# Kernel tuning notes

Measured on AMD Instinct MI355X. Metric: run time of the kernel, lower is better.

## Reference

```python
import jax, jax.numpy as jnp
import numpy as np

D = 64          # graph size d
HID = 1024      # hidden_dim of drift/diffusion MLPs


def _mlp(A_flat, t_val, W1, b1, W2, b2):
    """MLP over flattened adjacency concatenated with scalar time. A_flat: (..., d*d)."""
    t_col = jnp.full(A_flat.shape[:-1] + (1,), t_val, dtype=A_flat.dtype)
    x = jnp.concatenate([A_flat, t_col], axis=-1)          # (..., d*d+1)
    h = jnp.tanh(x @ W1 + b1)                              # (..., HID)
    return h @ W2 + b2                                     # (..., d*d)


def setup_inputs() -> dict:
    key = jax.random.key(0)
    ks = jax.random.split(key, 12)
    B, T = 64, 64
    A0 = jax.random.normal(ks[0], (B, D, D), dtype=jnp.float32)
    t = jnp.arange(T, dtype=jnp.float32) * 0.01
    din = D * D + 1
    s1 = 1.0 / np.sqrt(din)
    s2 = 1.0 / np.sqrt(HID)
    W1f = jax.random.normal(ks[1], (din, HID), jnp.float32) * s1
    b1f = jnp.zeros((HID,), jnp.float32)
    W2f = jax.random.normal(ks[2], (HID, D * D), jnp.float32) * s2
    b2f = jnp.zeros((D * D,), jnp.float32)
    W1g = jax.random.normal(ks[3], (din, HID), jnp.float32) * s1
    b1g = jnp.zeros((HID,), jnp.float32)
    W2g = jax.random.normal(ks[4], (HID, D * D), jnp.float32) * s2
    b2g = jnp.zeros((D * D,), jnp.float32)
    return dict(A0=A0, t=t, W1f=W1f, b1f=b1f, W2f=W2f, b2f=b2f,
                W1g=W1g, b1g=b1g, W2g=W2g, b2g=b2g, num_samples=4)


def reference(A0, t, W1f, b1f, W2f, b2f, W1g, b1g, W2g, b2g, num_samples):
    S = num_samples
    B = A0.shape[0]
    T = t.shape[0]
    dt = t[1] - t[0]
    sqrt_dt = jnp.sqrt(dt)
    A_init = jnp.broadcast_to(A0[None], (S, B, D, D))
    noise_keys = jax.random.split(jax.random.key(42), T - 1)

    def step(A_prev, inp):
        t_prev, k = inp
        Af = A_prev.reshape(S, B, D * D)
        drift = _mlp(Af, t_prev, W1f, b1f, W2f, b2f).reshape(S, B, D, D)
        diffusion = jax.nn.softplus(_mlp(Af, t_prev, W1g, b1g, W2g, b2g)).reshape(S, B, D, D)
        # torch draws dW with shape (*batch, d, d): shared across num_samples
        dW = jax.random.normal(k, (B, D, D), dtype=A_prev.dtype) * sqrt_dt
        A_next = A_prev + drift * dt + diffusion * dW
        return A_next, A_next

    _, traj = jax.lax.scan(step, A_init, (t[:-1], noise_keys))   # (T-1, S, B, d, d)
    A = jnp.concatenate([A_init[None], traj], axis=0)            # (T, S, B, d, d)
    A = jnp.swapaxes(A, 0, 1)                                    # (S, T, B, d, d)
    # ThresholdedSigmoid in training mode + zeroed diagonal
    G = jax.nn.sigmoid(A) * (1.0 - jnp.eye(D, dtype=A.dtype))
    return G
```

## Files before the change

### kernel.cpp

```cpp
#include <hip/hip_runtime.h>
#include <cstdint>

using u16 = unsigned short;
using u32 = uint32_t;
using u64 = unsigned long long;

typedef __bf16 bf16x8 __attribute__((ext_vector_type(8)));
typedef float  f32x4  __attribute__((ext_vector_type(4)));
typedef u32    uvec4  __attribute__((ext_vector_type(4)));

typedef const __attribute__((address_space(1))) void GV;
typedef __attribute__((address_space(3))) void LV;

#define MFMA(a, b, c) __builtin_amdgcn_mfma_f32_16x16x32_bf16((a), (b), (c), 0, 0, 0)
#define SCOPE_AGT __HIP_MEMORY_SCOPE_AGENT

static __device__ __forceinline__ void gl_lds16(const u16* g, u16* l) {
  __builtin_amdgcn_global_load_lds((GV*)g, (LV*)l, 16, 0, 0);
}
static __device__ __forceinline__ void st_dev(u64* p, u64 v) {
  __hip_atomic_store(p, v, __ATOMIC_RELAXED, SCOPE_AGT);
}

static __device__ __forceinline__ u16 f2bf(float x) {
  u32 u = __float_as_uint(x);
  u32 r = (u + 0x7FFFu + ((u >> 16) & 1u)) >> 16;
  return (u16)r;
}

static __device__ __forceinline__ u32 rotl32(u32 v, int s) {
  return (v << s) | (v >> (32 - s));
}

static __device__ __forceinline__ void threefry2x32(u32 k0, u32 k1, u32 x0, u32 x1,
                                                    u32& o0, u32& o1) {
  u32 k2 = k0 ^ k1 ^ 0x1BD11BDAu;
  x0 += k0; x1 += k1;
  x0 += x1; x1 = rotl32(x1, 13); x1 ^= x0;
  x0 += x1; x1 = rotl32(x1, 15); x1 ^= x0;
  x0 += x1; x1 = rotl32(x1, 26); x1 ^= x0;
  x0 += x1; x1 = rotl32(x1, 6);  x1 ^= x0;
  x0 += k1; x1 += k2 + 1u;
  x0 += x1; x1 = rotl32(x1, 17); x1 ^= x0;
  x0 += x1; x1 = rotl32(x1, 29); x1 ^= x0;
  x0 += x1; x1 = rotl32(x1, 16); x1 ^= x0;
  x0 += x1; x1 = rotl32(x1, 24); x1 ^= x0;
  x0 += k2; x1 += k0 + 2u;
  x0 += x1; x1 = rotl32(x1, 13); x1 ^= x0;
  x0 += x1; x1 = rotl32(x1, 15); x1 ^= x0;
  x0 += x1; x1 = rotl32(x1, 26); x1 ^= x0;
  x0 += x1; x1 = rotl32(x1, 6);  x1 ^= x0;
  x0 += k0; x1 += k1 + 3u;
  x0 += x1; x1 = rotl32(x1, 17); x1 ^= x0;
  x0 += x1; x1 = rotl32(x1, 29); x1 ^= x0;
  x0 += x1; x1 = rotl32(x1, 16); x1 ^= x0;
  x0 += x1; x1 = rotl32(x1, 24); x1 ^= x0;
  x0 += k1; x1 += k2 + 4u;
  x0 += x1; x1 = rotl32(x1, 13); x1 ^= x0;
  x0 += x1; x1 = rotl32(x1, 15); x1 ^= x0;
  x0 += x1; x1 = rotl32(x1, 26); x1 ^= x0;
  x0 += x1; x1 = rotl32(x1, 6);  x1 ^= x0;
  x0 += k2; x1 += k0 + 5u;
  o0 = x0; o1 = x1;
}

static __device__ __forceinline__ float bits_to_normal(u32 bits) {
  const float lo = __uint_as_float(0xBF7FFFFFu);
  float f = __uint_as_float((bits >> 9) | 0x3F800000u) - 1.0f;
  float x = fmaxf(lo, f * 2.0f + lo);
  float w = -logf((1.0f - x) * (1.0f + x));
  float p;
  if (w < 5.0f) {
    w -= 2.5f;
    p = 2.81022636e-08f;
    p = fmaf(p, w, 3.43273939e-07f);
    p = fmaf(p, w, -3.5233877e-06f);
    p = fmaf(p, w, -4.39150654e-06f);
    p = fmaf(p, w, 0.00021858087f);
    p = fmaf(p, w, -0.00125372503f);
    p = fmaf(p, w, -0.00417768164f);
    p = fmaf(p, w, 0.246640727f);
    p = fmaf(p, w, 1.50140941f);
  } else {
    w = sqrtf(w) - 3.0f;
    p = -0.000200214257f;
    p = fmaf(p, w, 0.000100950558f);
    p = fmaf(p, w, 0.00134934322f);
    p = fmaf(p, w, -0.00367342844f);
    p = fmaf(p, w, 0.00573950773f);
    p = fmaf(p, w, -0.0076224613f);
    p = fmaf(p, w, 0.00943887047f);
    p = fmaf(p, w, 1.00167406f);
    p = fmaf(p, w, 2.83297682f);
  }
  return 1.41421356f * p * x;
}

__global__ __launch_bounds__(256) void s1_frag(
    const float* __restrict__ W1f, const float* __restrict__ W1g,
    const float* __restrict__ W2f, const float* __restrict__ W2g,
    u16* __restrict__ W1P, u16* __restrict__ W2P) {
  const int gid = blockIdx.x * 256 + threadIdx.x;
  const int f = gid >> 6, l = gid & 63;
  const int lr = l & 15, kg = l >> 4;
  u32 wbuf[4];
  if (f < 16384) {
    const int net = f >> 13, r = f & 8191, ct = r >> 7, q = r & 127;
    const float* __restrict__ src = net ? W1g : W1f;
    const int k = q * 32 + kg * 8, c = ct * 16 + lr;
    #pragma unroll
    for (int p = 0; p < 4; ++p) {
      u16 e0 = f2bf(src[(size_t)(k + 2 * p) * 1024 + c]);
      u16 e1 = f2bf(src[(size_t)(k + 2 * p + 1) * 1024 + c]);
      wbuf[p] = (u32)e0 | ((u32)e1 << 16);
    }
    *(uvec4*)(W1P + (size_t)f * 512 + l * 8) = *(uvec4*)wbuf;
  } else {
    const int f2 = f - 16384;
    const int net = f2 >> 13, r = f2 & 8191, ct = r >> 5, q = r & 31;
    const float* __restrict__ src = net ? W2g : W2f;
    const int k = q * 32 + kg * 8, c = ct * 16 + lr;
    #pragma unroll
    for (int p = 0; p < 4; ++p) {
      u16 e0 = f2bf(src[(size_t)(k + 2 * p) * 4096 + c]);
      u16 e1 = f2bf(src[(size_t)(k + 2 * p + 1) * 4096 + c]);
      wbuf[p] = (u32)e0 | ((u32)e1 << 16);
    }
    *(uvec4*)(W2P + (size_t)f2 * 512 + l * 8) = *(uvec4*)wbuf;
  }
}

__global__ __launch_bounds__(256) void s2_init(
    const float* __restrict__ A0, u16* __restrict__ APack,
    u32* __restrict__ ctr, float* __restrict__ out) {
  const int gid = blockIdx.x * 256 + threadIdx.x;
  const int n = gid & 4095, b = gid >> 12;
  const float a0 = A0[gid];
  const float sig = (n % 65 == 0) ? 0.0f : 1.0f / (1.0f + expf(-a0));
  #pragma unroll
  for (int s = 0; s < 4; ++s)
    out[((size_t)(s * 64) * 64 + b) * 4096 + n] = sig;
  if (gid < 32768) {
    const int fr = gid >> 6, l = gid & 63;
    const int m = fr >> 7, q = fr & 127;
    const int row = m * 16 + (l & 15);
    const int k = q * 32 + (l >> 4) * 8;
    u32 wbuf[4];
    #pragma unroll
    for (int p = 0; p < 4; ++p) {
      u16 e0 = f2bf(A0[(size_t)row * 4096 + k + 2 * p]);
      u16 e1 = f2bf(A0[(size_t)row * 4096 + k + 2 * p + 1]);
      wbuf[p] = (u32)e0 | ((u32)e1 << 16);
    }
    *(uvec4*)(APack + (size_t)fr * 512 + l * 8) = *(uvec4*)wbuf;
  }
  if (gid < 2048) ctr[gid] = 0;
}

static __device__ __forceinline__ void half_barrier(u32* ctr, int mp, int g, u32 tag) {
  __syncthreads();
  if (threadIdx.x == 0) {
    u32* arr  = ctr + (mp * 20 + g) * 32;
    u32* glob = ctr + (mp * 20 + 8) * 32;
    u32* flg  = ctr + (mp * 20 + 9 + g) * 32;
    u32 old = __hip_atomic_fetch_add(arr, 1u, __ATOMIC_RELAXED, SCOPE_AGT);
    if (old + 1u == 16u * tag) {
      u32 go = __hip_atomic_fetch_add(glob, 1u, __ATOMIC_RELAXED, SCOPE_AGT);
      if (go + 1u == 8u * tag) {
        #pragma unroll
        for (int i = 0; i < 8; ++i)
          __hip_atomic_store(ctr + (mp * 20 + 9 + i) * 32, tag, __ATOMIC_RELAXED, SCOPE_AGT);
      }
    }
    while (__hip_atomic_load(flg, __ATOMIC_RELAXED, SCOPE_AGT) < tag)
      __builtin_amdgcn_s_sleep(8);
  }
  __syncthreads();
}

__global__ __launch_bounds__(512) void sde_fused(
    const float* __restrict__ A0, const float* __restrict__ tarr,
    const u16* __restrict__ W1P, const u16* __restrict__ W2P,
    const float* __restrict__ b1f, const float* __restrict__ b1g,
    const float* __restrict__ W1fv, const float* __restrict__ W1gv,
    const float* __restrict__ b2f, const float* __restrict__ b2g,
    u16* __restrict__ APack, u16* __restrict__ HPack,
    u32* __restrict__ ctr, float* __restrict__ out) {
  extern __shared__ __align__(16) char smraw[];
  u16* w2l = (u16*)smraw;
  char* exraw = smraw + 131072;
  f32x4 (*paex)[64]     = (f32x4 (*)[64])exraw;
  u16 (*patile)[16][16] = (u16 (*)[16][16])(exraw + 8192);
  f32x4 (*pbex)[64][2]  = (f32x4 (*)[64][2])exraw;
  u16 (*pbtile)[16][32] = (u16 (*)[16][32])(exraw + 16384);
  uint2* dwk = (uint2*)(exraw + 18432);

  const int bid = blockIdx.x, tix = threadIdx.x;
  const int wid = tix >> 6, lane = tix & 63;
  const int lr = lane & 15, lq = lane >> 4;
  const int mp = bid >> 7;
  const int ctF = bid & 127;
  const int netA = ctF >> 6, ctA = ctF & 63;
  const int mA = wid & 1, ksA = wid >> 1;
  const int mGA = mp * 2 + mA;
  const int ct32 = bid & 127;
  const int ksB = wid >> 2, netB = (wid >> 1) & 1, mB = wid & 1;
  const int mGB = mp * 2 + mB;
  const int eM = wid & 1, eCf = (wid >> 1) & 1, eRh = wid >> 2;
  const int nc = ct32 * 32 + eCf * 16 + lr;
  const int g = (bid & 127) >> 4;

  #pragma unroll
  for (int i = 0; i < 16; ++i) {
    const int f = wid * 16 + i;
    const int nf = f >> 6, cf = (f >> 5) & 1, ksf = (f >> 4) & 1, df = f & 15;
    const u16* src = W2P
        + ((size_t)((nf * 256 + ct32 * 2 + cf) * 32 + ksf * 16 + df)) * 512 + lane * 8;
    gl_lds16(src, w2l + (size_t)f * 512);
  }
  if (tix < 63) {
    u32 y0, y1;
    threefry2x32(0u, 42u, 0u, (u32)tix, y0, y1);
    dwk[tix] = make_uint2(y0, y1);
  }
  bf16x8 wv[32];
  {
    const u16* pw = W1P + ((size_t)((netA * 64 + ctA) * 128 + ksA * 32)) * 512 + lane * 8;
    #pragma unroll
    for (int d = 0; d < 32; ++d) wv[d] = *(const bf16x8*)(pw + (size_t)d * 512);
  }
  float Ast[2];
  #pragma unroll
  for (int ri = 0; ri < 2; ++ri) {
    const int row = mp * 32 + eM * 16 + lq * 4 + eRh * 2 + ri;
    Ast[ri] = A0[(size_t)row * 4096 + nc];
  }
  asm volatile("s_waitcnt vmcnt(0)" ::: "memory");
  __syncthreads();

  const float dt = tarr[1] - tarr[0];
  const float sdt = sqrtf(dt);

  for (int step = 0; step < 63; ++step) {
    {
      const u16* pa = APack + (size_t)step * 262144
                    + ((size_t)(mGA * 128 + ksA * 32)) * 512 + lane * 8;
      bf16x8 av[16];
      #pragma unroll
      for (int d = 0; d < 16; ++d) av[d] = *(const bf16x8*)(pa + (size_t)d * 512);
      f32x4 acc = {0.f, 0.f, 0.f, 0.f};
      #pragma unroll
      for (int j = 0; j < 32; ++j) {
        const int s = j & 15;
        acc = MFMA(av[s], wv[j], acc);
        if (j + 16 < 32) av[s] = *(const bf16x8*)(pa + (size_t)(j + 16) * 512);
      }
      paex[wid][lane] = acc;
      __syncthreads();
      {
        const int gM = wid & 1, gR = wid >> 1;
        const f32x4 s0 = paex[gM][lane];
        const f32x4 s1 = paex[2 + gM][lane];
        const f32x4 s2 = paex[4 + gM][lane];
        const f32x4 s3 = paex[6 + gM][lane];
        const float ch = s0[gR] + s1[gR] + s2[gR] + s3[gR];
        const int ncl = ctA * 16 + lr;
        const float* __restrict__ b1 = netA ? b1g : b1f;
        const float* __restrict__ wl = (netA ? W1gv : W1fv) + (size_t)4096 * 1024;
        const float cc = b1[ncl] + tarr[step] * wl[ncl];
        patile[gM][lq * 4 + gR][lr] = f2bf(tanhf(ch + cc));
      }
      __syncthreads();
      if (wid < 2 && lane < 32) {
        const int mm = wid;
        const int row = lane & 15, kp = lane >> 4;
        const u16* src = &patile[mm][row][kp * 8];
        const u64 lo = *(const u64*)src;
        const u64 hi = *(const u64*)(src + 4);
        const int k8 = (ctA & 1) * 2 + kp;
        u16* dst = HPack + (size_t)step * 131072
                 + ((size_t)((netA * 4 + mp * 2 + mm) * 32 + (ctA >> 1))) * 512
                 + (k8 * 16 + row) * 8;
        st_dev((u64*)dst, lo);
        st_dev((u64*)dst + 1, hi);
      }
      asm volatile("s_waitcnt vmcnt(0)" ::: "memory");
      half_barrier(ctr, mp, g, 2u * (u32)step + 1u);
    }

    {
      const u16* ph = HPack + (size_t)step * 131072
                    + ((size_t)((netB * 4 + mGB) * 32 + ksB * 16)) * 512 + lane * 8;
      bf16x8 hv[8];
      #pragma unroll
      for (int d = 0; d < 8; ++d) hv[d] = *(const bf16x8*)(ph + (size_t)d * 512);
      const u16* wl0 = w2l + (size_t)(netB * 64 + ksB * 16) * 512 + lane * 8;
      const u16* wl1 = wl0 + (size_t)32 * 512;
      f32x4 a0 = {0.f, 0.f, 0.f, 0.f}, a1 = a0;
      #pragma unroll
      for (int j = 0; j < 16; ++j) {
        const int s = j & 7;
        const bf16x8 w0 = *(const bf16x8*)(wl0 + (size_t)j * 512);
        const bf16x8 w1 = *(const bf16x8*)(wl1 + (size_t)j * 512);
        a0 = MFMA(hv[s], w0, a0);
        a1 = MFMA(hv[s], w1, a1);
        if (j + 8 < 16) hv[s] = *(const bf16x8*)(ph + (size_t)(j + 8) * 512);
      }
      pbex[wid][lane][0] = a0;
      pbex[wid][lane][1] = a1;
      __syncthreads();
      float sg[2];
      {
        const f32x4 CF = pbex[eM][lane][eCf] + pbex[4 + eM][lane][eCf];
        const f32x4 CG = pbex[2 + eM][lane][eCf] + pbex[6 + eM][lane][eCf];
        const float bfv = b2f[nc], bgv = b2g[nc];
        const uint2 key = dwk[step];
        #pragma unroll
        for (int ri = 0; ri < 2; ++ri) {
          const int r = eRh * 2 + ri;
          const int row = mp * 32 + eM * 16 + lq * 4 + r;
          const float drift = CF[r] + bfv;
          const float graw = CG[r] + bgv;
          const float diff = fmaxf(graw, 0.0f) + log1pf(expf(-fabsf(graw)));
          u32 y0, y1;
          threefry2x32(key.x, key.y, 0u, (u32)(row * 4096 + nc), y0, y1);
          const float dw = bits_to_normal(y0 ^ y1) * sdt;
          const float an = Ast[ri] + drift * dt + diff * dw;
          Ast[ri] = an;
          pbtile[eM][lq * 4 + r][eCf * 16 + lr] = f2bf(an);
          sg[ri] = (nc % 65 == 0) ? 0.0f : 1.0f / (1.0f + expf(-an));
        }
      }
      __syncthreads();
      if (wid < 2) {
        const int mm = wid;
        const int row = lane & 15, kq = lane >> 4;
        const u16* src = &pbtile[mm][row][kq * 8];
        const u64 lo = *(const u64*)src;
        const u64 hi = *(const u64*)(src + 4);
        u16* dst = APack + (size_t)(step + 1) * 262144
                 + ((size_t)((mp * 2 + mm) * 128 + ct32)) * 512 + lane * 8;
        st_dev((u64*)dst, lo);
        st_dev((u64*)dst + 1, hi);
      }
      asm volatile("s_waitcnt vmcnt(0)" ::: "memory");
      #pragma unroll
      for (int ri = 0; ri < 2; ++ri) {
        const int row = mp * 32 + eM * 16 + lq * 4 + eRh * 2 + ri;
        #pragma unroll
        for (int s = 0; s < 4; ++s)
          __builtin_nontemporal_store(
              sg[ri], &out[((size_t)(s * 64 + step + 1) * 64 + row) * 4096 + nc]);
      }
      if (step < 62) half_barrier(ctr, mp, g, 2u * (u32)step + 2u);
    }
  }
}

extern "C" void kernel_launch(void* const* d_in, const int* in_sizes, int n_in,
                              void* d_out, int out_size, void* d_ws, size_t ws_size,
                              hipStream_t stream) {
  const float* A0 = (const float*)d_in[0];
  const float* tarr = (const float*)d_in[1];
  const float* W1f = (const float*)d_in[2];
  const float* b1f = (const float*)d_in[3];
  const float* W2f = (const float*)d_in[4];
  const float* b2f = (const float*)d_in[5];
  const float* W1g = (const float*)d_in[6];
  const float* b1g = (const float*)d_in[7];
  const float* W2g = (const float*)d_in[8];
  const float* b2g = (const float*)d_in[9];
  float* outp = (float*)d_out;
  char* ws = (char*)d_ws;
  const size_t MB = 1024 * 1024;
  u16* W1P   = (u16*)(ws + 0 * MB);
  u16* W2P   = (u16*)(ws + 16 * MB);
  u16* APack = (u16*)(ws + 32 * MB);
  u16* HPack = (u16*)(ws + 64 * MB);
  u32* ctr   = (u32*)(ws + 80 * MB);

  s1_frag<<<dim3(8192), 256, 0, stream>>>(W1f, W1g, W2f, W2g, W1P, W2P);
  s2_init<<<dim3(1024), 256, 0, stream>>>(A0, APack, ctr, outp);

  void* kargs[] = {
    (void*)&A0, (void*)&tarr,
    (void*)&W1P, (void*)&W2P,
    (void*)&b1f, (void*)&b1g, (void*)&W1f, (void*)&W1g,
    (void*)&b2f, (void*)&b2g,
    (void*)&APack, (void*)&HPack, (void*)&ctr, (void*)&outp
  };
  hipLaunchCooperativeKernel((const void*)sde_fused, dim3(256), dim3(512),
                             kargs, 150016, stream);
}
```

Measured before the change: 795.9 us.

## Replace group barriers with per-dependency counters and split MFMA accumulators

Drops the two-level half_barrier. Each block now bumps an arrival counter after publishing its tile, and before the next phase it waits only on the two counters for the producer groups whose data it actually reads. Output stores are moved after the arrival signal, the per-step bias and time-weight loads are hoisted out of the loop, and the first GEMM alternates between two accumulators to shorten the MFMA dependency chain. The intent is to cut global synchronisation latency and let blocks run ahead, but correctness now rests on the counter indexing and memory ordering being exact.

```diff
diff --git a/kernel.cpp b/kernel.cpp
--- a/kernel.cpp
+++ b/kernel.cpp
@@ -20,6 +20,12 @@
 }
 static __device__ __forceinline__ void st_dev(u64* p, u64 v) {
   __hip_atomic_store(p, v, __ATOMIC_RELAXED, SCOPE_AGT);
+}
+static __device__ __forceinline__ void wait_pair(const u32* base, u32 tag) {
+  while (__hip_atomic_load(base, __ATOMIC_RELAXED, SCOPE_AGT) < tag)
+    __builtin_amdgcn_s_sleep(2);
+  while (__hip_atomic_load(base + 32, __ATOMIC_RELAXED, SCOPE_AGT) < tag)
+    __builtin_amdgcn_s_sleep(2);
 }
 
 static __device__ __forceinline__ u16 f2bf(float x) {
@@ -157,27 +163,6 @@
   if (gid < 2048) ctr[gid] = 0;
 }
 
-static __device__ __forceinline__ void half_barrier(u32* ctr, int mp, int g, u32 tag) {
-  __syncthreads();
-  if (threadIdx.x == 0) {
-    u32* arr  = ctr + (mp * 20 + g) * 32;
-    u32* glob = ctr + (mp * 20 + 8) * 32;
-    u32* flg  = ctr + (mp * 20 + 9 + g) * 32;
-    u32 old = __hip_atomic_fetch_add(arr, 1u, __ATOMIC_RELAXED, SCOPE_AGT);
-    if (old + 1u == 16u * tag) {
-      u32 go = __hip_atomic_fetch_add(glob, 1u, __ATOMIC_RELAXED, SCOPE_AGT);
-      if (go + 1u == 8u * tag) {
-        #pragma unroll
-        for (int i = 0; i < 8; ++i)
-          __hip_atomic_store(ctr + (mp * 20 + 9 + i) * 32, tag, __ATOMIC_RELAXED, SCOPE_AGT);
-      }
-    }
-    while (__hip_atomic_load(flg, __ATOMIC_RELAXED, SCOPE_AGT) < tag)
-      __builtin_amdgcn_s_sleep(8);
-  }
-  __syncthreads();
-}
-
 __global__ __launch_bounds__(512) void sde_fused(
     const float* __restrict__ A0, const float* __restrict__ tarr,
     const u16* __restrict__ W1P, const u16* __restrict__ W2P,
@@ -208,7 +193,11 @@
   const int mGB = mp * 2 + mB;
   const int eM = wid & 1, eCf = (wid >> 1) & 1, eRh = wid >> 2;
   const int nc = ct32 * 32 + eCf * 16 + lr;
-  const int g = (bid & 127) >> 4;
+  const int g = ctF >> 4;
+  u32* arrA = ctr + (mp * 8 + g) * 32;
+  u32* arrB = ctr + (16 + mp * 8 + g) * 32;
+  const u32* waitA = ctr + (16 + mp * 8 + ksA * 2) * 32;
+  const u32* waitB = ctr + (mp * 8 + netB * 4 + ksB * 2) * 32;
 
   #pragma unroll
   for (int i = 0; i < 16; ++i) {
@@ -235,6 +224,11 @@
     const int row = mp * 32 + eM * 16 + lq * 4 + eRh * 2 + ri;
     Ast[ri] = A0[(size_t)row * 4096 + nc];
   }
+  const int nclA = ctA * 16 + lr;
+  const float bAc = (netA ? b1g : b1f)[nclA];
+  const float wAc = ((netA ? W1gv : W1fv) + (size_t)4096 * 1024)[nclA];
+  const float bfv = b2f[nc], bgv = b2g[nc];
+  const bool diag0 = (nc % 65 == 0);
   asm volatile("s_waitcnt vmcnt(0)" ::: "memory");
   __syncthreads();
 
@@ -243,19 +237,21 @@
 
   for (int step = 0; step < 63; ++step) {
     {
+      wait_pair(waitA, 16u * (u32)step);
       const u16* pa = APack + (size_t)step * 262144
                     + ((size_t)(mGA * 128 + ksA * 32)) * 512 + lane * 8;
       bf16x8 av[16];
       #pragma unroll
       for (int d = 0; d < 16; ++d) av[d] = *(const bf16x8*)(pa + (size_t)d * 512);
-      f32x4 acc = {0.f, 0.f, 0.f, 0.f};
+      f32x4 acc0 = {0.f, 0.f, 0.f, 0.f}, acc1 = acc0;
       #pragma unroll
       for (int j = 0; j < 32; ++j) {
         const int s = j & 15;
-        acc = MFMA(av[s], wv[j], acc);
+        if (j & 1) acc1 = MFMA(av[s], wv[j], acc1);
+        else       acc0 = MFMA(av[s], wv[j], acc0);
         if (j + 16 < 32) av[s] = *(const bf16x8*)(pa + (size_t)(j + 16) * 512);
       }
-      paex[wid][lane] = acc;
+      paex[wid][lane] = acc0 + acc1;
       __syncthreads();
       {
         const int gM = wid & 1, gR = wid >> 1;
@@ -264,10 +260,7 @@
         const f32x4 s2 = paex[4 + gM][lane];
         const f32x4 s3 = paex[6 + gM][lane];
         const float ch = s0[gR] + s1[gR] + s2[gR] + s3[gR];
-        const int ncl = ctA * 16 + lr;
-        const float* __restrict__ b1 = netA ? b1g : b1f;
-        const float* __restrict__ wl = (netA ? W1gv : W1fv) + (size_t)4096 * 1024;
-        const float cc = b1[ncl] + tarr[step] * wl[ncl];
+        const float cc = bAc + tarr[step] * wAc;
         patile[gM][lq * 4 + gR][lr] = f2bf(tanhf(ch + cc));
       }
       __syncthreads();
@@ -285,10 +278,13 @@
         st_dev((u64*)dst + 1, hi);
       }
       asm volatile("s_waitcnt vmcnt(0)" ::: "memory");
-      half_barrier(ctr, mp, g, 2u * (u32)step + 1u);
+      __syncthreads();
+      if (tix == 0)
+        __hip_atomic_fetch_add(arrA, 1u, __ATOMIC_RELAXED, SCOPE_AGT);
     }
 
     {
+      wait_pair(waitB, 16u * (u32)(step + 1));
       const u16* ph = HPack + (size_t)step * 131072
                     + ((size_t)((netB * 4 + mGB) * 32 + ksB * 16)) * 512 + lane * 8;
       bf16x8 hv[8];
@@ -313,7 +309,6 @@
       {
         const f32x4 CF = pbex[eM][lane][eCf] + pbex[4 + eM][lane][eCf];
         const f32x4 CG = pbex[2 + eM][lane][eCf] + pbex[6 + eM][lane][eCf];
-        const float bfv = b2f[nc], bgv = b2g[nc];
         const uint2 key = dwk[step];
         #pragma unroll
         for (int ri = 0; ri < 2; ++ri) {
@@ -328,7 +323,7 @@
           const float an = Ast[ri] + drift * dt + diff * dw;
           Ast[ri] = an;
           pbtile[eM][lq * 4 + r][eCf * 16 + lr] = f2bf(an);
-          sg[ri] = (nc % 65 == 0) ? 0.0f : 1.0f / (1.0f + expf(-an));
+          sg[ri] = diag0 ? 0.0f : 1.0f / (1.0f + expf(-an));
         }
       }
       __syncthreads();
@@ -344,6 +339,9 @@
         st_dev((u64*)dst + 1, hi);
       }
       asm volatile("s_waitcnt vmcnt(0)" ::: "memory");
+      __syncthreads();
+      if (tix == 0)
+        __hip_atomic_fetch_add(arrB, 1u, __ATOMIC_RELAXED, SCOPE_AGT);
       #pragma unroll
       for (int ri = 0; ri < 2; ++ri) {
         const int row = mp * 32 + eM * 16 + lq * 4 + eRh * 2 + ri;
@@ -352,7 +350,6 @@
           __builtin_nontemporal_store(
               sg[ri], &out[((size_t)(s * 64 + step + 1) * 64 + row) * 4096 + nc]);
       }
-      if (step < 62) half_barrier(ctr, mp, g, 2u * (u32)step + 2u);
     }
   }
 }
```

Result: slower. 930.8 us (+16.9%).
